# Optimization experiments

Measured on AMD Instinct MI355X. Metric: run time of the kernel, lower is better.

The kernel has to match this reference:

```python
import jax, jax.numpy as jnp
import numpy as np

N = 50000      # n_nodes
E = 600000     # n_edges (avg degree 12)
IN_DIM = 128
HID = 256
OUT = 2


def _glorot(k, fan_in, fan_out):
    s = jnp.sqrt(6.0 / (fan_in + fan_out))
    return jax.random.uniform(k, (fan_in, fan_out), jnp.float32, -s, s)


def setup_inputs() -> dict:
    key = jax.random.key(0)
    ks = jax.random.split(key, 6)
    x = jax.random.normal(ks[0], (N, IN_DIM), jnp.float32)
    edge_index = jax.random.randint(ks[1], (2, E), 0, N, jnp.int32)
    W1 = _glorot(ks[2], IN_DIM, HID)
    b1 = jnp.zeros((HID,), jnp.float32)
    W2 = _glorot(ks[3], HID, HID)
    b2 = jnp.zeros((HID,), jnp.float32)
    Wl = _glorot(ks[4], HID, OUT)
    bl = jnp.zeros((OUT,), jnp.float32)
    return {"x": x, "edge_index": edge_index, "W1": W1, "b1": b1,
            "W2": W2, "b2": b2, "Wl": Wl, "bl": bl}


def _gcn_conv(x, W, b, src, dst, dinv, n):
    # PyG GCNConv: transform, then propagate with symmetric norm + self-loops.
    h = x @ W                                   # [N, F_out]
    norm = (dinv[src] * dinv[dst])[:, None]     # [E, 1]
    agg = jax.ops.segment_sum(h[src] * norm, dst, num_segments=n)
    agg = agg + h * (dinv * dinv)[:, None]      # self-loop term: deg^-1 * h
    return agg + b


def reference(x, edge_index, W1, b1, W2, b2, Wl, bl):
    n = x.shape[0]
    src, dst = edge_index[0], edge_index[1]
    # degree (with self-loop) computed on destination nodes, as in PyG gcn_norm
    deg = jax.ops.segment_sum(jnp.ones((src.shape[0],), jnp.float32), dst,
                              num_segments=n) + 1.0
    dinv = jax.lax.rsqrt(deg)
    h = jax.nn.relu(_gcn_conv(x, W1, b1, src, dst, dinv, n))
    # dropout is identity in eval mode
    h = jax.nn.relu(_gcn_conv(h, W2, b2, src, dst, dinv, n))
    return h @ Wl + bl
```

## Files before the change

kernel.cpp:

```cpp
#include <hip/hip_runtime.h>
#include <hip/hip_bf16.h>
#include <hip/hip_fp16.h>

constexpr int IN_DIM = 128;
constexpr int HID    = 256;

typedef _Float16 f16x8 __attribute__((ext_vector_type(8)));
typedef float    f32x4 __attribute__((ext_vector_type(4)));


__global__ void zero_int2(int* __restrict__ a, int* __restrict__ b, int n) {
    int i = blockIdx.x * blockDim.x + threadIdx.x;
    if (i < n) { a[i] = 0; b[i] = 0; }
}

__global__ void count_deg(const int* __restrict__ dst, int* __restrict__ deg, int e) {
    int i = blockIdx.x * blockDim.x + threadIdx.x;
    if (i < e) atomicAdd(&deg[dst[i]], 1);
}

__global__ __launch_bounds__(256) void scan_partial(const int* __restrict__ deg,
                                                    int* __restrict__ escan,
                                                    int* __restrict__ blocksum,
                                                    float* __restrict__ dinv, int n) {
    __shared__ int lds[256];
    int t = threadIdx.x;
    int i = blockIdx.x * 256 + t;
    int v = (i < n) ? deg[i] : 0;
    if (i < n) dinv[i] = rsqrtf((float)v + 1.0f);
    lds[t] = v;
    __syncthreads();
    for (int off = 1; off < 256; off <<= 1) {
        int a = lds[t];
        int w = (t >= off) ? lds[t - off] : 0;
        __syncthreads();
        lds[t] = a + w;
        __syncthreads();
    }
    if (i < n) escan[i] = lds[t] - v;
    if (t == 255) blocksum[blockIdx.x] = lds[255];
}

__global__ __launch_bounds__(256) void scan_rest(const int* __restrict__ escan,
                                                 const int* __restrict__ blocksum,
                                                 int nb, int* __restrict__ rowptr, int n) {
    __shared__ int lds[256];
    int t = threadIdx.x;
    int v = (t < nb) ? blocksum[t] : 0;
    lds[t] = v;
    __syncthreads();
    for (int off = 1; off < 256; off <<= 1) {
        int a = lds[t];
        int w = (t >= off) ? lds[t - off] : 0;
        __syncthreads();
        lds[t] = a + w;
        __syncthreads();
    }
    int boff = (blockIdx.x > 0) ? lds[blockIdx.x - 1] : 0;
    int i = blockIdx.x * 256 + t;
    if (i < n) rowptr[i] = escan[i] + boff;
    if (blockIdx.x == 0 && t == 0) rowptr[n] = lds[nb - 1];
}

__global__ void scatter_edges(const int* __restrict__ src, const int* __restrict__ dst,
                              const int* __restrict__ rowptr, int* __restrict__ cursor,
                              const float* __restrict__ dinv,
                              int* __restrict__ ssrc, float* __restrict__ ewt, int e) {
    int i = blockIdx.x * blockDim.x + threadIdx.x;
    if (i < e) {
        int d = dst[i];
        int s = src[i];
        int p = atomicAdd(&cursor[d], 1);
        int idx = rowptr[d] + p;
        ssrc[idx] = s;
        ewt[idx]  = dinv[s] * dinv[d];
    }
}

__device__ inline void conv_B_elem(const float* B, ushort* Bp, int id, int ) {
    int k  = id >> 6;
    int n4 = (id & 63) * 4;
    float4 v = *(const float4*)(B + (size_t)k * 256 + n4);
    size_t base = (size_t)(k >> 5) * (256 * 32) + (k & 31);
    Bp[base + (size_t)(n4 + 0) * 32] = __half_as_ushort(__float2half(v.x));
    Bp[base + (size_t)(n4 + 1) * 32] = __half_as_ushort(__float2half(v.y));
    Bp[base + (size_t)(n4 + 2) * 32] = __half_as_ushort(__float2half(v.z));
    Bp[base + (size_t)(n4 + 3) * 32] = __half_as_ushort(__float2half(v.w));
}

__global__ void convert_inputs(const float* __restrict__ W1, ushort* __restrict__ B1p,
                               const float* __restrict__ W2, ushort* __restrict__ B2p,
                               const float* __restrict__ x, ushort* __restrict__ xh,
                               int total4) {
    int id = blockIdx.x * 256 + threadIdx.x;
    if (id < IN_DIM * 64) {
        conv_B_elem(W1, B1p, id, IN_DIM);
    } else if (id < IN_DIM * 64 + HID * 64) {
        conv_B_elem(W2, B2p, id - IN_DIM * 64, HID);
    } else {
        int i = id - (IN_DIM * 64 + HID * 64);
        if (i < total4) {
            float4 v = *(const float4*)(x + (size_t)i * 4);
            ushort4 o;
            o.x = __half_as_ushort(__float2half(v.x));
            o.y = __half_as_ushort(__float2half(v.y));
            o.z = __half_as_ushort(__float2half(v.z));
            o.w = __half_as_ushort(__float2half(v.w));
            *(ushort4*)(xh + (size_t)i * 4) = o;
        }
    }
}

template <int K>
__global__ __launch_bounds__(256) void aggregate_p(const ushort* __restrict__ h,
                                                   const int* __restrict__ rowptr,
                                                   const int* __restrict__ ssrc,
                                                   const float* __restrict__ ewt,
                                                   const float* __restrict__ dinv,
                                                   ushort* __restrict__ Pp,
                                                   int n, int Mp) {
    constexpr int VH = K / 64;
    int wid  = (blockIdx.x * 256 + threadIdx.x) >> 6;
    int lane = threadIdx.x & 63;
    if (wid >= n) return;
    float di = dinv[wid];
    float sw = di * di;
    float acc[VH];
    {
        const ushort* row = h + (size_t)wid * K + lane * VH;
        if constexpr (VH == 4) {
            uint2 u = *(const uint2*)row;
            float2 fa = __half22float2(*(__half2*)&u.x);
            float2 fb = __half22float2(*(__half2*)&u.y);
            acc[0] = fa.x * sw; acc[1] = fa.y * sw; acc[2] = fb.x * sw; acc[3] = fb.y * sw;
        } else {
            uint u = *(const uint*)row;
            float2 fa = __half22float2(*(__half2*)&u);
            acc[0] = fa.x * sw; acc[1] = fa.y * sw;
        }
    }
    int beg = rowptr[wid], fin = rowptr[wid + 1];
    for (int b = beg; b < fin; b += 64) {
        int cnt = fin - b;
        if (cnt > 64) cnt = 64;
        int   sv = (lane < cnt) ? ssrc[b + lane] : 0;
        float wv = (lane < cnt) ? ewt[b + lane]  : 0.f;
        int t = 0;
        for (; t + 8 <= cnt; t += 8) {
            float wr[8];
            if constexpr (VH == 4) {
                uint2 u[8];
#pragma unroll
                for (int k = 0; k < 8; k++) {
                    int s = __shfl(sv, t + k);
                    wr[k] = __shfl(wv, t + k);
                    u[k] = *(const uint2*)(h + (size_t)s * K + lane * VH);
                }
#pragma unroll
                for (int k = 0; k < 8; k++) {
                    float2 fa = __half22float2(*(__half2*)&u[k].x);
                    float2 fb = __half22float2(*(__half2*)&u[k].y);
                    acc[0] += fa.x * wr[k]; acc[1] += fa.y * wr[k];
                    acc[2] += fb.x * wr[k]; acc[3] += fb.y * wr[k];
                }
            } else {
                uint u[8];
#pragma unroll
                for (int k = 0; k < 8; k++) {
                    int s = __shfl(sv, t + k);
                    wr[k] = __shfl(wv, t + k);
                    u[k] = *(const uint*)(h + (size_t)s * K + lane * VH);
                }
#pragma unroll
                for (int k = 0; k < 8; k++) {
                    float2 fa = __half22float2(*(__half2*)&u[k]);
                    acc[0] += fa.x * wr[k]; acc[1] += fa.y * wr[k];
                }
            }
        }
        for (; t + 4 <= cnt; t += 4) {
            float wr[4];
            if constexpr (VH == 4) {
                uint2 u[4];
#pragma unroll
                for (int k = 0; k < 4; k++) {
                    int s = __shfl(sv, t + k);
                    wr[k] = __shfl(wv, t + k);
                    u[k] = *(const uint2*)(h + (size_t)s * K + lane * VH);
                }
#pragma unroll
                for (int k = 0; k < 4; k++) {
                    float2 fa = __half22float2(*(__half2*)&u[k].x);
                    float2 fb = __half22float2(*(__half2*)&u[k].y);
                    acc[0] += fa.x * wr[k]; acc[1] += fa.y * wr[k];
                    acc[2] += fb.x * wr[k]; acc[3] += fb.y * wr[k];
                }
            } else {
                uint u[4];
#pragma unroll
                for (int k = 0; k < 4; k++) {
                    int s = __shfl(sv, t + k);
                    wr[k] = __shfl(wv, t + k);
                    u[k] = *(const uint*)(h + (size_t)s * K + lane * VH);
                }
#pragma unroll
                for (int k = 0; k < 4; k++) {
                    float2 fa = __half22float2(*(__half2*)&u[k]);
                    acc[0] += fa.x * wr[k]; acc[1] += fa.y * wr[k];
                }
            }
        }
        for (; t < cnt; t++) {
            int   s = __shfl(sv, t);
            float w = __shfl(wv, t);
            const ushort* r = h + (size_t)s * K + lane * VH;
            if constexpr (VH == 4) {
                uint2 u = *(const uint2*)r;
                float2 fa = __half22float2(*(__half2*)&u.x);
                float2 fb = __half22float2(*(__half2*)&u.y);
                acc[0] += fa.x * w; acc[1] += fa.y * w;
                acc[2] += fb.x * w; acc[3] += fb.y * w;
            } else {
                uint u = *(const uint*)r;
                float2 fa = __half22float2(*(__half2*)&u);
                acc[0] += fa.x * w; acc[1] += fa.y * w;
            }
        }
    }
    int kglob = lane * VH;
    int chunk = kglob >> 5;
    int inner = kglob & 31;
    size_t base = (size_t)chunk * Mp * 32 + (size_t)wid * 32 + inner;
    if constexpr (VH == 4) {
        __half2 p0 = __floats2half2_rn(acc[0], acc[1]);
        __half2 p1 = __floats2half2_rn(acc[2], acc[3]);
        *(uint2*)&Pp[base] = make_uint2(*(uint*)&p0, *(uint*)&p1);
    } else {
        __half2 p0 = __floats2half2_rn(acc[0], acc[1]);
        *(uint*)&Pp[base] = *(uint*)&p0;
    }
}

template <int K, int MODE>
__global__ __launch_bounds__(256, 4) void gemm_f16(const ushort* __restrict__ Ap,
                                                   const ushort* __restrict__ Bp,
                                                   const float* __restrict__ bias,
                                                   ushort* __restrict__ C16,
                                                   const float* __restrict__ Wl,
                                                   const float* __restrict__ bl,
                                                   float* __restrict__ out,
                                                   int M, int Mp) {
    constexpr int NC = K / 32;
    __shared__ ushort Asm[NC * 1024];
    __shared__ float part[4][32][2];

    int tid  = threadIdx.x;
    int w    = tid >> 6;
    int lane = tid & 63;
    int l15  = lane & 15;
    int quad = lane >> 4;
    int row0 = blockIdx.x * 32;

    constexpr int TOT = NC * 2;
    for (int j = w; j < TOT; j += 4) {
        int c   = j >> 1;
        int sub = j & 1;
        const ushort* g = Ap + (size_t)c * Mp * 32 + (size_t)(row0 + sub * 16) * 32;
        ushort* l = Asm + c * 1024 + sub * 512;
        __builtin_amdgcn_global_load_lds(
            (const __attribute__((address_space(1))) uint*)(g + (size_t)lane * 8),
            (__attribute__((address_space(3))) uint*)l, 16, 0, 0);
    }
    __syncthreads();

    size_t bco[4];
#pragma unroll
    for (int j = 0; j < 4; j++) bco[j] = (size_t)(w * 64 + j * 16 + l15) * 32 + quad * 8;

    f16x8 fb[2][4];
    auto loadB = [&](int c, int buf) {
        const ushort* bp = Bp + (size_t)c * 256 * 32;
#pragma unroll
        for (int j = 0; j < 4; j++) fb[buf][j] = *(const f16x8*)(bp + bco[j]);
    };

    f32x4 acc[2][4] = {};
    loadB(0, 0);
#pragma unroll
    for (int c = 0; c < NC; c++) {
        int cur = c & 1;
        if (c + 1 < NC) loadB(c + 1, cur ^ 1);
        f16x8 fa[2];
#pragma unroll
        for (int i = 0; i < 2; i++) {
            int off = c * 1024 + (i * 16 + l15) * 32 + quad * 8;
            fa[i] = *(const f16x8*)&Asm[off];
        }
#pragma unroll
        for (int i = 0; i < 2; i++)
#pragma unroll
            for (int j = 0; j < 4; j++)
                acc[i][j] = __builtin_amdgcn_mfma_f32_16x16x32_f16(fa[i], fb[cur][j], acc[i][j], 0, 0, 0);
    }

    float bj[4];
#pragma unroll
    for (int j = 0; j < 4; j++) bj[j] = bias[w * 64 + j * 16 + l15];

    if constexpr (MODE == 1) {
#pragma unroll
        for (int i = 0; i < 2; i++)
#pragma unroll
            for (int reg = 0; reg < 4; reg++) {
                int r = row0 + i * 16 + quad * 4 + reg;
                if (r < M) {
                    ushort* cp = C16 + (size_t)r * 256 + w * 64 + l15;
#pragma unroll
                    for (int j = 0; j < 4; j++) {
                        float v = fmaxf(acc[i][j][reg] + bj[j], 0.f);
                        cp[j * 16] = __half_as_ushort(__float2half(v));
                    }
                }
            }
    } else {
        float wl0[4], wl1[4];
#pragma unroll
        for (int j = 0; j < 4; j++) {
            int cj = w * 64 + j * 16 + l15;
            float2 wv = *(const float2*)(Wl + cj * 2);
            wl0[j] = wv.x; wl1[j] = wv.y;
        }
#pragma unroll
        for (int i = 0; i < 2; i++)
#pragma unroll
            for (int reg = 0; reg < 4; reg++) {
                float s0 = 0.f, s1 = 0.f;
#pragma unroll
                for (int j = 0; j < 4; j++) {
                    float v = fmaxf(acc[i][j][reg] + bj[j], 0.f);
                    s0 += v * wl0[j];
                    s1 += v * wl1[j];
                }
#pragma unroll
                for (int off = 1; off < 16; off <<= 1) {
                    s0 += __shfl_xor(s0, off);
                    s1 += __shfl_xor(s1, off);
                }
                if (l15 == 0) {
                    int r = i * 16 + quad * 4 + reg;
                    part[w][r][0] = s0;
                    part[w][r][1] = s1;
                }
            }
        __syncthreads();
        if (tid < 64) {
            int r = tid >> 1, o = tid & 1;
            int grr = row0 + r;
            if (grr < M) {
                float s = part[0][r][o] + part[1][r][o] + part[2][r][o] + part[3][r][o] + bl[o];
                out[(size_t)grr * 2 + o] = s;
            }
        }
    }
}


extern "C" void kernel_launch(void* const* d_in, const int* in_sizes, int n_in,
                              void* d_out, int out_size, void* d_ws, size_t ws_size,
                              hipStream_t stream) {
    const float* x  = (const float*)d_in[0];
    const int*   ei = (const int*)d_in[1];
    const float* W1 = (const float*)d_in[2];
    const float* b1 = (const float*)d_in[3];
    const float* W2 = (const float*)d_in[4];
    const float* b2 = (const float*)d_in[5];
    const float* Wl = (const float*)d_in[6];
    const float* bl = (const float*)d_in[7];
    float* out = (float*)d_out;

    int n = in_sizes[0] / IN_DIM;
    int e = in_sizes[1] / 2;
    const int* src = ei;
    const int* dst = ei + e;

    int gblocks = (n + 31) / 32;
    int Mp = gblocks * 32;

    char* ws = (char*)d_ws;
    size_t off = 0;
    auto alloc = [&](size_t bytes) -> void* {
        void* p = ws + off;
        off += (bytes + 255) & ~(size_t)255;
        return p;
    };
    int*    deg    = (int*)alloc((size_t)n * 4);
    int*    cursor = (int*)alloc((size_t)n * 4);
    float*  dinv   = (float*)alloc((size_t)n * 4);
    int*    rowptr = (int*)alloc((size_t)(n + 1) * 4);
    int*    escan  = (int*)alloc((size_t)n * 4);
    int*    bsum   = (int*)alloc(256 * 4);
    int*    ssrc   = (int*)alloc((size_t)e * 4);
    float*  ewt    = (float*)alloc((size_t)e * 4);
    ushort* xh     = (ushort*)alloc((size_t)n * IN_DIM * 2);
    ushort* h1     = (ushort*)alloc((size_t)n * HID * 2);
    ushort* A1p    = (ushort*)alloc((size_t)Mp * IN_DIM * 2);
    ushort* A2p    = (ushort*)alloc((size_t)Mp * HID * 2);
    ushort* B1p    = (ushort*)alloc((size_t)IN_DIM * 256 * 2);
    ushort* B2p    = (ushort*)alloc((size_t)HID * 256 * 2);

    int nb = (n + 255) / 256;
    int eb = (e + 255) / 256;

    zero_int2<<<nb, 256, 0, stream>>>(deg, cursor, n);
    count_deg<<<eb, 256, 0, stream>>>(dst, deg, e);

    scan_partial<<<nb, 256, 0, stream>>>(deg, escan, bsum, dinv, n);
    scan_rest<<<nb, 256, 0, stream>>>(escan, bsum, nb, rowptr, n);

    scatter_edges<<<eb, 256, 0, stream>>>(src, dst, rowptr, cursor, dinv, ssrc, ewt, e);

    int total4 = n * IN_DIM / 4;
    int cblocks = (IN_DIM * 64 + HID * 64 + total4 + 255) / 256;
    convert_inputs<<<cblocks, 256, 0, stream>>>(W1, B1p, W2, B2p, x, xh, total4);

    aggregate_p<IN_DIM><<<(n + 3) / 4, 256, 0, stream>>>(xh, rowptr, ssrc, ewt, dinv,
                                                         A1p, n, Mp);
    gemm_f16<IN_DIM, 1><<<gblocks, 256, 0, stream>>>(A1p, B1p, b1, h1,
                                                     nullptr, nullptr, nullptr, n, Mp);

    aggregate_p<HID><<<(n + 3) / 4, 256, 0, stream>>>(h1, rowptr, ssrc, ewt, dinv,
                                                      A2p, n, Mp);
    gemm_f16<HID, 2><<<gblocks, 256, 0, stream>>>(A2p, B2p, b2, nullptr,
                                                  Wl, bl, out, n, Mp);
}
```

Baseline: 256.8 us.

## Stage GEMM B tiles through LDS and fold zeroing into the convert kernel

The GEMM kernel now loads the weight matrix B into a double-buffered shared-memory tile with async global-to-LDS loads, one K chunk per iteration with a barrier each step, instead of loading B fragments directly from global memory into registers. Occupancy is lowered to 3 blocks per SM to fit the extra 32 KB of LDS. Separately, the deg/cursor zeroing kernel is merged into convert_inputs, which moves ahead of count_deg to remove one launch. The per-chunk barriers and lower occupancy may offset the gain from reading B through LDS.

```diff
diff --git a/kernel.cpp b/kernel.cpp
--- a/kernel.cpp
+++ b/kernel.cpp
@@ -8,11 +8,6 @@
 typedef _Float16 f16x8 __attribute__((ext_vector_type(8)));
 typedef float    f32x4 __attribute__((ext_vector_type(4)));
 
-
-__global__ void zero_int2(int* __restrict__ a, int* __restrict__ b, int n) {
-    int i = blockIdx.x * blockDim.x + threadIdx.x;
-    if (i < n) { a[i] = 0; b[i] = 0; }
-}
 
 __global__ void count_deg(const int* __restrict__ dst, int* __restrict__ deg, int e) {
     int i = blockIdx.x * blockDim.x + threadIdx.x;
@@ -77,7 +72,7 @@
     }
 }
 
-__device__ inline void conv_B_elem(const float* B, ushort* Bp, int id, int ) {
+__device__ inline void conv_B_elem(const float* B, ushort* Bp, int id) {
     int k  = id >> 6;
     int n4 = (id & 63) * 4;
     float4 v = *(const float4*)(B + (size_t)k * 256 + n4);
@@ -91,23 +86,27 @@
 __global__ void convert_inputs(const float* __restrict__ W1, ushort* __restrict__ B1p,
                                const float* __restrict__ W2, ushort* __restrict__ B2p,
                                const float* __restrict__ x, ushort* __restrict__ xh,
-                               int total4) {
+                               int total4, int* __restrict__ deg,
+                               int* __restrict__ cursor, int n) {
     int id = blockIdx.x * 256 + threadIdx.x;
-    if (id < IN_DIM * 64) {
-        conv_B_elem(W1, B1p, id, IN_DIM);
-    } else if (id < IN_DIM * 64 + HID * 64) {
-        conv_B_elem(W2, B2p, id - IN_DIM * 64, HID);
+    constexpr int C1 = IN_DIM * 64;
+    constexpr int C2 = C1 + HID * 64;
+    if (id < C1) {
+        conv_B_elem(W1, B1p, id);
+    } else if (id < C2) {
+        conv_B_elem(W2, B2p, id - C1);
+    } else if (id < C2 + total4) {
+        int i = id - C2;
+        float4 v = *(const float4*)(x + (size_t)i * 4);
+        ushort4 o;
+        o.x = __half_as_ushort(__float2half(v.x));
+        o.y = __half_as_ushort(__float2half(v.y));
+        o.z = __half_as_ushort(__float2half(v.z));
+        o.w = __half_as_ushort(__float2half(v.w));
+        *(ushort4*)(xh + (size_t)i * 4) = o;
     } else {
-        int i = id - (IN_DIM * 64 + HID * 64);
-        if (i < total4) {
-            float4 v = *(const float4*)(x + (size_t)i * 4);
-            ushort4 o;
-            o.x = __half_as_ushort(__float2half(v.x));
-            o.y = __half_as_ushort(__float2half(v.y));
-            o.z = __half_as_ushort(__float2half(v.z));
-            o.w = __half_as_ushort(__float2half(v.w));
-            *(ushort4*)(xh + (size_t)i * 4) = o;
-        }
+        int i = id - (C2 + total4);
+        if (i < n) { deg[i] = 0; cursor[i] = 0; }
     }
 }
 
@@ -242,7 +241,7 @@
 }
 
 template <int K, int MODE>
-__global__ __launch_bounds__(256, 4) void gemm_f16(const ushort* __restrict__ Ap,
+__global__ __launch_bounds__(256, 3) void gemm_f16(const ushort* __restrict__ Ap,
                                                    const ushort* __restrict__ Bp,
                                                    const float* __restrict__ bias,
                                                    ushort* __restrict__ C16,
@@ -252,6 +251,7 @@
                                                    int M, int Mp) {
     constexpr int NC = K / 32;
     __shared__ ushort Asm[NC * 1024];
+    __shared__ ushort Bsm[2][8192];
     __shared__ float part[4][32][2];
 
     int tid  = threadIdx.x;
@@ -261,8 +261,8 @@
     int quad = lane >> 4;
     int row0 = blockIdx.x * 32;
 
-    constexpr int TOT = NC * 2;
-    for (int j = w; j < TOT; j += 4) {
+    constexpr int TOTA = NC * 2;
+    for (int j = w; j < TOTA; j += 4) {
         int c   = j >> 1;
         int sub = j & 1;
         const ushort* g = Ap + (size_t)c * Mp * 32 + (size_t)(row0 + sub * 16) * 32;
@@ -271,36 +271,48 @@
             (const __attribute__((address_space(1))) uint*)(g + (size_t)lane * 8),
             (__attribute__((address_space(3))) uint*)l, 16, 0, 0);
     }
-    __syncthreads();
-
-    size_t bco[4];
-#pragma unroll
-    for (int j = 0; j < 4; j++) bco[j] = (size_t)(w * 64 + j * 16 + l15) * 32 + quad * 8;
-
-    f16x8 fb[2][4];
-    auto loadB = [&](int c, int buf) {
-        const ushort* bp = Bp + (size_t)c * 256 * 32;
-#pragma unroll
-        for (int j = 0; j < 4; j++) fb[buf][j] = *(const f16x8*)(bp + bco[j]);
-    };
+#pragma unroll
+    for (int j = 0; j < 4; j++) {
+        int seg = w * 4 + j;
+        const ushort* g = Bp + (size_t)seg * 512;
+        ushort* l = Bsm[0] + seg * 512;
+        __builtin_amdgcn_global_load_lds(
+            (const __attribute__((address_space(1))) uint*)(g + (size_t)lane * 8),
+            (__attribute__((address_space(3))) uint*)l, 16, 0, 0);
+    }
 
     f32x4 acc[2][4] = {};
-    loadB(0, 0);
 #pragma unroll
     for (int c = 0; c < NC; c++) {
-        int cur = c & 1;
-        if (c + 1 < NC) loadB(c + 1, cur ^ 1);
-        f16x8 fa[2];
+        __syncthreads();
+        if (c + 1 < NC) {
+            int nb_ = (c + 1) & 1;
+#pragma unroll
+            for (int j = 0; j < 4; j++) {
+                int seg = w * 4 + j;
+                const ushort* g = Bp + (size_t)(c + 1) * 8192 + (size_t)seg * 512;
+                ushort* l = Bsm[nb_] + seg * 512;
+                __builtin_amdgcn_global_load_lds(
+                    (const __attribute__((address_space(1))) uint*)(g + (size_t)lane * 8),
+                    (__attribute__((address_space(3))) uint*)l, 16, 0, 0);
+            }
+        }
+        f16x8 fa[2], fb[4];
 #pragma unroll
         for (int i = 0; i < 2; i++) {
             int off = c * 1024 + (i * 16 + l15) * 32 + quad * 8;
             fa[i] = *(const f16x8*)&Asm[off];
         }
 #pragma unroll
+        for (int j = 0; j < 4; j++) {
+            int off = (w * 64 + j * 16 + l15) * 32 + quad * 8;
+            fb[j] = *(const f16x8*)&Bsm[c & 1][off];
+        }
+#pragma unroll
         for (int i = 0; i < 2; i++)
 #pragma unroll
             for (int j = 0; j < 4; j++)
-                acc[i][j] = __builtin_amdgcn_mfma_f32_16x16x32_f16(fa[i], fb[cur][j], acc[i][j], 0, 0, 0);
+                acc[i][j] = __builtin_amdgcn_mfma_f32_16x16x32_f16(fa[i], fb[j], acc[i][j], 0, 0, 0);
     }
 
     float bj[4];
@@ -411,17 +423,15 @@
     int nb = (n + 255) / 256;
     int eb = (e + 255) / 256;
 
-    zero_int2<<<nb, 256, 0, stream>>>(deg, cursor, n);
+    int total4 = n * IN_DIM / 4;
+    int citems = IN_DIM * 64 + HID * 64 + total4 + n;
+    convert_inputs<<<(citems + 255) / 256, 256, 0, stream>>>(W1, B1p, W2, B2p, x, xh,
+                                                             total4, deg, cursor, n);
+
     count_deg<<<eb, 256, 0, stream>>>(dst, deg, e);
-
     scan_partial<<<nb, 256, 0, stream>>>(deg, escan, bsum, dinv, n);
     scan_rest<<<nb, 256, 0, stream>>>(escan, bsum, nb, rowptr, n);
-
     scatter_edges<<<eb, 256, 0, stream>>>(src, dst, rowptr, cursor, dinv, ssrc, ewt, e);
-
-    int total4 = n * IN_DIM / 4;
-    int cblocks = (IN_DIM * 64 + HID * 64 + total4 + 255) / 256;
-    convert_inputs<<<cblocks, 256, 0, stream>>>(W1, B1p, W2, B2p, x, xh, total4);
 
     aggregate_p<IN_DIM><<<(n + 3) / 4, 256, 0, stream>>>(xh, rowptr, ssrc, ewt, dinv,
                                                          A1p, n, Mp);
```

New measurement: 254.8 us. Within noise of the previous version (-0.8%).
